# Performance work log

Measured on AMD Instinct MI355X. Metric: run time of the kernel, lower is better.

Reference implementation:

```python
import jax, jax.numpy as jnp
import numpy as np

N_NODES = 10000
N_EDGES = 320000
H = 256
L = 3
EPS = 1e-5


def _mlp2(x, w1, b1, w2, b2):
    # Linear -> ReLU -> Linear
    return jax.nn.relu(x @ w1 + b1) @ w2 + b2


def _layer_norm(x, g, b):
    mu = jnp.mean(x, axis=-1, keepdims=True)
    var = jnp.var(x, axis=-1, keepdims=True)
    return (x - mu) * jax.lax.rsqrt(var + EPS) * g + b


def setup_inputs() -> dict:
    key = jax.random.key(0)
    ks = jax.random.split(key, 24)
    s = 0.02
    inp = {
        "node_features": jax.random.normal(ks[0], (N_NODES, H), dtype=jnp.float32),
        "edge_index": jax.random.randint(ks[1], (2, N_EDGES), 0, N_NODES, dtype=jnp.int64),
        # node encoder (Linear 256->256, ReLU, Linear 256->256)
        "ne_w1": jax.random.normal(ks[2], (H, H), dtype=jnp.float32) * s,
        "ne_b1": jnp.zeros((H,), jnp.float32),
        "ne_w2": jax.random.normal(ks[3], (H, H), dtype=jnp.float32) * s,
        "ne_b2": jnp.zeros((H,), jnp.float32),
        # per-layer message MLP (2H->H, ReLU, H->H), stacked over L layers
        "msg_w1": jax.random.normal(ks[4], (L, 2 * H, H), dtype=jnp.float32) * s,
        "msg_b1": jnp.zeros((L, H), jnp.float32),
        "msg_w2": jax.random.normal(ks[5], (L, H, H), dtype=jnp.float32) * s,
        "msg_b2": jnp.zeros((L, H), jnp.float32),
        # per-layer update MLP (2H->H, ReLU, H->H)
        "upd_w1": jax.random.normal(ks[6], (L, 2 * H, H), dtype=jnp.float32) * s,
        "upd_b1": jnp.zeros((L, H), jnp.float32),
        "upd_w2": jax.random.normal(ks[7], (L, H, H), dtype=jnp.float32) * s,
        "upd_b2": jnp.zeros((L, H), jnp.float32),
        # per-layer LayerNorm
        "ln_g": jnp.ones((L, H), jnp.float32),
        "ln_b": jnp.zeros((L, H), jnp.float32),
        # readout MLP
        "ro_w1": jax.random.normal(ks[8], (H, H), dtype=jnp.float32) * s,
        "ro_b1": jnp.zeros((H,), jnp.float32),
        "ro_w2": jax.random.normal(ks[9], (H, H), dtype=jnp.float32) * s,
        "ro_b2": jnp.zeros((H,), jnp.float32),
    }
    return inp


def reference(node_features, edge_index, ne_w1, ne_b1, ne_w2, ne_b2,
              msg_w1, msg_b1, msg_w2, msg_b2,
              upd_w1, upd_b1, upd_w2, upd_b2,
              ln_g, ln_b, ro_w1, ro_b1, ro_w2, ro_b2):
    n_nodes = node_features.shape[0]
    src, dst = edge_index[0], edge_index[1]

    # node encoder
    x = _mlp2(node_features, ne_w1, ne_b1, ne_w2, ne_b2)  # [N, H]

    # message passing layers (edge_attr is unused in the original layer)
    for l in range(L):
        cat_e = jnp.concatenate([x[src], x[dst]], axis=-1)          # [E, 2H]
        messages = _mlp2(cat_e, msg_w1[l], msg_b1[l], msg_w2[l], msg_b2[l])  # [E, H]
        aggregated = jax.ops.segment_sum(messages, dst, num_segments=n_nodes)  # [N, H]
        cat_n = jnp.concatenate([x, aggregated], axis=-1)           # [N, 2H]
        updated = _mlp2(cat_n, upd_w1[l], upd_b1[l], upd_w2[l], upd_b2[l])
        x = _layer_norm(x + updated, ln_g[l], ln_b[l])

    # mean readout
    g = jnp.mean(x, axis=0)  # [H]
    return _mlp2(g, ro_w1, ro_b1, ro_w2, ro_b2)  # [H]
```

## Files before the change

### kernel.cpp

```cpp
#include <hip/hip_runtime.h>

#define NN 10000
#define NE 320000
#define HD 256
#define NL 3

typedef unsigned short ushort_t;
typedef __attribute__((ext_vector_type(8))) short bf16x8;
typedef __attribute__((ext_vector_type(4))) float f32x4;

#define MFMA __builtin_amdgcn_mfma_f32_16x16x32_bf16

#define WAITV(N) asm volatile("s_waitcnt vmcnt(" #N ")" ::: "memory")
#define SCHEDPIN() __builtin_amdgcn_sched_barrier(0)
#define LGKMBAR() do { asm volatile("s_waitcnt lgkmcnt(0)" ::: "memory"); \
                       __builtin_amdgcn_s_barrier(); __builtin_amdgcn_sched_barrier(0); } while (0)

__device__ __forceinline__ unsigned short f2bf(float x) {
    unsigned u = __float_as_uint(x);
    unsigned rounding = 0x7FFFu + ((u >> 16) & 1u);
    return (unsigned short)((u + rounding) >> 16);
}
__device__ __forceinline__ float bf2f(unsigned short u) {
    return __uint_as_float(((unsigned)u) << 16);
}
__device__ __forceinline__ int sw2(int col) { return (col & 3) ^ ((col >> 2) & 3); }
__device__ __forceinline__ void dma16(const void* g, void* l) {
    __builtin_amdgcn_global_load_lds(
        (const __attribute__((address_space(1))) unsigned int*)g,
        (__attribute__((address_space(3))) unsigned int*)l, 16, 0, 0);
}


__global__ void hist_deg(const int* __restrict__ dst, int* __restrict__ deg, int E) {
    int e = blockIdx.x * blockDim.x + threadIdx.x;
    if (e < E) atomicAdd(&deg[dst[e]], 1);
}

__global__ __launch_bounds__(1024) void scan_csr(const int* __restrict__ deg,
                                                 int* __restrict__ row_start,
                                                 int* __restrict__ cursor,
                                                 float* __restrict__ degf,
                                                 float* __restrict__ gsum, int n) {
    __shared__ int wsum[16];
    __shared__ int carry_s;
    int tid = threadIdx.x, lane = tid & 63, wid = tid >> 6;
    if (tid < HD) gsum[tid] = 0.f;
    if (tid == 0) carry_s = 0;
    __syncthreads();
    for (int base = 0; base < n; base += 1024) {
        int i = base + tid;
        int v = (i < n) ? deg[i] : 0;
        int s = v;
        #pragma unroll
        for (int off = 1; off < 64; off <<= 1) {
            int t = __shfl_up(s, off);
            if (lane >= off) s += t;
        }
        if (lane == 63) wsum[wid] = s;
        __syncthreads();
        if (wid == 0 && lane < 16) {
            int ws = wsum[lane];
            #pragma unroll
            for (int off = 1; off < 16; off <<= 1) {
                int t = __shfl_up(ws, off);
                if (lane >= off) ws += t;
            }
            wsum[lane] = ws;
        }
        __syncthreads();
        int carry = carry_s;
        int wpre = (wid > 0) ? wsum[wid - 1] : 0;
        int incl = carry + wpre + s;
        int excl = incl - v;
        if (i < n) { row_start[i] = excl; cursor[i] = excl; degf[i] = (float)v; }
        __syncthreads();
        if (tid == 1023) carry_s = incl;
        __syncthreads();
    }
    if (tid == 0) row_start[n] = carry_s;
}

__global__ void scatter_src(const int* __restrict__ src, const int* __restrict__ dst,
                            int* __restrict__ cursor, int* __restrict__ src_sorted, int E) {
    int e = blockIdx.x * blockDim.x + threadIdx.x;
    if (e < E) {
        int pos = atomicAdd(&cursor[dst[e]], 1);
        src_sorted[pos] = src[e];
    }
}


struct TDesc { const float* src; ushort_t* dst; int mode; };
struct TArgs { TDesc d[20]; };

__global__ __launch_bounds__(256) void conv_t(TArgs args) {
    __shared__ ushort_t tile[64][65];
    const float* src = args.d[blockIdx.y].src;
    ushort_t* dst = args.d[blockIdx.y].dst;
    int mode = args.d[blockIdx.y].mode;
    int t = blockIdx.x;
    int r0 = (t >> 2) * 64, c0 = (t & 3) * 64;
    int tid = threadIdx.x;
    int rr = tid >> 4, cc4 = (tid & 15) * 4;
    if (mode == 0) {
        #pragma unroll
        for (int i = 0; i < 4; ++i) {
            int r = r0 + rr + i * 16;
            float4 v = *(const float4*)(src + (size_t)r * HD + c0 + cc4);
            ushort4 o = { f2bf(v.x), f2bf(v.y), f2bf(v.z), f2bf(v.w) };
            *(ushort4*)(dst + (size_t)r * HD + c0 + cc4) = o;
        }
        return;
    }
    #pragma unroll
    for (int i = 0; i < 4; ++i) {
        int r = rr + i * 16;
        float4 v = *(const float4*)(src + (size_t)(r0 + r) * HD + c0 + cc4);
        tile[cc4 + 0][r] = f2bf(v.x);
        tile[cc4 + 1][r] = f2bf(v.y);
        tile[cc4 + 2][r] = f2bf(v.z);
        tile[cc4 + 3][r] = f2bf(v.w);
    }
    __syncthreads();
    #pragma unroll
    for (int i = 0; i < 4; ++i) {
        int c = rr + i * 16;
        ushort4 o = { tile[c][cc4], tile[c][cc4 + 1], tile[c][cc4 + 2], tile[c][cc4 + 3] };
        if (mode == 1) {
            *(ushort4*)(dst + (size_t)(c0 + c) * HD + r0 + cc4) = o;
        } else {
            int col = c0 + c;
            int k = r0 + cc4;
            int s = k >> 5, qv = (k >> 3) & 3;
            int slot = qv ^ sw2(col);
            *(ushort4*)(dst + (size_t)s * 8192 + col * 32 + slot * 8 + (k & 7)) = o;
        }
    }
}

__global__ __launch_bounds__(256) void cast_nf_tiled(const float* __restrict__ src,
                                                     ushort_t* __restrict__ dst) {
    int blk = blockIdx.x;
    int row = threadIdx.x >> 4, g = threadIdx.x & 15;
    const float* sp = src + ((size_t)blk * 16 + row) * HD + g * 16;
    ushort_t* dp = dst + (size_t)blk * 4096 + (g >> 1) * 512 + row * 32 + (g & 1) * 16;
    #pragma unroll
    for (int j = 0; j < 4; ++j) {
        float4 v = *(const float4*)(sp + j * 4);
        ushort4 o = { f2bf(v.x), f2bf(v.y), f2bf(v.z), f2bf(v.w) };
        *(ushort4*)(dp + j * 4) = o;
    }
}

__global__ __launch_bounds__(256) void bias_compose(const float* __restrict__ mb2,
                                                    const float* __restrict__ uw1,
                                                    float* __restrict__ out) {
    int l = blockIdx.x, c = threadIdx.x;
    const float* b2l = mb2 + (size_t)l * HD;
    const float* u1b = uw1 + (size_t)l * 2 * HD * HD + (size_t)HD * HD;
    float s = 0.f;
    for (int k = 0; k < HD; ++k) s += b2l[k] * u1b[(size_t)k * HD + c];
    out[(size_t)l * HD + c] = s;
}

__global__ __launch_bounds__(256) void gemm_w2u(
    const ushort_t* __restrict__ Abase, const ushort_t* __restrict__ Btbase,
    ushort_t* __restrict__ outBase)
{
    const ushort_t* A  = Abase  + (size_t)blockIdx.z * HD * HD;
    const ushort_t* Bt = Btbase + (size_t)blockIdx.z * HD * HD;
    ushort_t* outB     = outBase + (size_t)blockIdx.z * HD * HD;
    int tid = threadIdx.x;
    int wid = tid >> 6, lane = tid & 63;
    int wm = wid >> 1, wn = wid & 1;
    int row0 = blockIdx.x * 64 + wm * 32;
    int col0 = blockIdx.y * 64 + wn * 32;
    int lm = lane & 15, lk = (lane >> 4) * 8;
    f32x4 acc[2][2] = {};
    const ushort_t* a0p = A + (size_t)(row0 + lm) * HD + lk;
    const ushort_t* a1p = A + (size_t)(row0 + 16 + lm) * HD + lk;
    const ushort_t* b0p = Bt + (size_t)(col0 + lm) * HD + lk;
    const ushort_t* b1p = Bt + (size_t)(col0 + 16 + lm) * HD + lk;
    #pragma unroll
    for (int k0 = 0; k0 < HD; k0 += 32) {
        bf16x8 a0 = *(const bf16x8*)(a0p + k0);
        bf16x8 a1 = *(const bf16x8*)(a1p + k0);
        bf16x8 b0 = *(const bf16x8*)(b0p + k0);
        bf16x8 b1 = *(const bf16x8*)(b1p + k0);
        acc[0][0] = MFMA(a0, b0, acc[0][0], 0, 0, 0);
        acc[0][1] = MFMA(a0, b1, acc[0][1], 0, 0, 0);
        acc[1][0] = MFMA(a1, b0, acc[1][0], 0, 0, 0);
        acc[1][1] = MFMA(a1, b1, acc[1][1], 0, 0, 0);
    }
    int orow = (lane >> 4) * 4;
    #pragma unroll
    for (int mi = 0; mi < 2; ++mi)
        #pragma unroll
        for (int r = 0; r < 4; ++r) {
            int row = row0 + mi * 16 + orow + r;
            #pragma unroll
            for (int ni = 0; ni < 2; ++ni) {
                int col = col0 + ni * 16 + lm;
                int s = col >> 5, qv = (col >> 3) & 3;
                int slot = qv ^ sw2(row);
                outB[(size_t)s * 8192 + row * 32 + slot * 8 + (col & 7)] = f2bf(acc[mi][ni][r]);
            }
        }
}

__device__ __forceinline__ int swz(int row, int byte_in_row) {
    return row * 512 + (byte_in_row ^ ((row & 7) << 4));
}


__global__ __launch_bounds__(512, 4) void enc_pq(
    const ushort_t* __restrict__ Anf, const ushort_t* __restrict__ B1t,
    const ushort_t* __restrict__ B2t,
    const float* __restrict__ b1, const float* __restrict__ b2,
    const ushort_t* __restrict__ Pw1t, const ushort_t* __restrict__ Pw1b,
    const float* __restrict__ pqb1,
    float* __restrict__ xF, ushort_t* __restrict__ xB,
    ushort_t* __restrict__ P, float* __restrict__ Q, int M)
{
    __shared__ char wlds[8][2][2][2048];
    __shared__ char hid[16 * 512];
    int tid = threadIdx.x;
    int w = tid >> 6, lane = tid & 63;
    int lm = lane & 15, q = lane >> 4;
    int row0 = blockIdx.x * 16;
    int col0 = w * 32;
    int cA = col0 + lm, cB = col0 + 16 + lm;

    auto stageW = [&](const ushort_t* Wt, int s, int p, int m) {
        #pragma unroll
        for (int i = 0; i < 2; ++i)
            dma16((const char*)Wt + (size_t)s * 16384 + (col0 + 16 * i) * 64 + lane * 16,
                  wlds[w][p][m] + i * 1024);
    };
    auto readB = [&](int p, int m, int ni) -> bf16x8 {
        int col = col0 + 16 * ni + lm;
        int q2 = q ^ sw2(col);
        return *(const bf16x8*)(wlds[w][p][m] + ni * 1024 + lm * 64 + q2 * 16);
    };

    float b1v[2] = { b1[cA], b1[cB] };
    float b2v[2] = { b2[cA], b2[cB] };
    float pqv[2] = { pqb1[cA], pqb1[cB] };

    const ushort_t* ap = Anf + (size_t)blockIdx.x * 4096 + lm * 32 + q * 8;
    bf16x8 ax[2];
    #pragma unroll
    for (int s = 0; s < 2; ++s) {
        stageW(B1t, s, s, 0);
        ax[s] = *(const bf16x8*)(ap + s * 512);
        SCHEDPIN();
    }

    f32x4 acc[2] = {};
    #pragma unroll
    for (int j = 0; j < 8; ++j) {
        int p = j & 1;
        if (j < 7) { WAITV(3); } else { WAITV(0); }
        acc[0] = MFMA(ax[p], readB(p, 0, 0), acc[0], 0, 0, 0);
        acc[1] = MFMA(ax[p], readB(p, 0, 1), acc[1], 0, 0, 0);
        SCHEDPIN();
        if (j < 6) {
            stageW(B1t, j + 2, p, 0);
            ax[p] = *(const bf16x8*)(ap + (j + 2) * 512);
            SCHEDPIN();
        }
    }

    #pragma unroll
    for (int s = 0; s < 2; ++s) { stageW(B2t, s, s, 0); SCHEDPIN(); }
    #pragma unroll
    for (int ni = 0; ni < 2; ++ni) {
        int col = col0 + 16 * ni + lm;
        #pragma unroll
        for (int r = 0; r < 4; ++r) {
            int row = 4 * q + r;
            float v = fmaxf(acc[ni][r] + b1v[ni], 0.f);
            *(ushort_t*)(hid + swz(row, col * 2)) = f2bf(v);
        }
    }
    LGKMBAR();

    f32x4 acc2[2] = {};
    #pragma unroll
    for (int j = 0; j < 8; ++j) {
        int p = j & 1;
        if (j < 7) { WAITV(2); } else { WAITV(0); }
        int bk = (j * 32 + q * 8) * 2;
        bf16x8 a = *(const bf16x8*)(hid + swz(lm, bk));
        acc2[0] = MFMA(a, readB(p, 0, 0), acc2[0], 0, 0, 0);
        acc2[1] = MFMA(a, readB(p, 0, 1), acc2[1], 0, 0, 0);
        SCHEDPIN();
        if (j < 6) { stageW(B2t, j + 2, p, 0); SCHEDPIN(); }
    }

    #pragma unroll
    for (int s = 0; s < 2; ++s) {
        stageW(Pw1t, s, s, 0);
        stageW(Pw1b, s, s, 1);
        SCHEDPIN();
    }
    LGKMBAR();
    int tbase = blockIdx.x * 4096 + w * 512;
    #pragma unroll
    for (int ni = 0; ni < 2; ++ni) {
        int col = col0 + 16 * ni + lm;
        #pragma unroll
        for (int r = 0; r < 4; ++r) {
            int row = 4 * q + r;
            int grow = row0 + row;
            float v = acc2[ni][r] + b2v[ni];
            *(ushort_t*)(hid + swz(row, col * 2)) = f2bf(v);
            xF[(size_t)grow * HD + col] = v;
            xB[tbase + row * 32 + 16 * ni + lm] = f2bf(v);
        }
    }
    LGKMBAR();

    f32x4 aP[2] = {}, aQ[2] = {};
    #pragma unroll
    for (int j = 0; j < 8; ++j) {
        int p = j & 1;
        if (j < 7) { WAITV(4); } else { WAITV(0); }
        int bk = (j * 32 + q * 8) * 2;
        bf16x8 a = *(const bf16x8*)(hid + swz(lm, bk));
        #pragma unroll
        for (int ni = 0; ni < 2; ++ni) {
            aP[ni] = MFMA(a, readB(p, 0, ni), aP[ni], 0, 0, 0);
            aQ[ni] = MFMA(a, readB(p, 1, ni), aQ[ni], 0, 0, 0);
        }
        SCHEDPIN();
        if (j < 6) {
            stageW(Pw1t, j + 2, p, 0);
            stageW(Pw1b, j + 2, p, 1);
            SCHEDPIN();
        }
    }
    #pragma unroll
    for (int r = 0; r < 4; ++r) {
        int grow = row0 + 4 * q + r;
        #pragma unroll
        for (int ni = 0; ni < 2; ++ni) {
            int col = col0 + 16 * ni + lm;
            P[(size_t)grow * HD + col] = f2bf(aP[ni][r]);
            Q[(size_t)grow * HD + col] = aQ[ni][r] + pqv[ni];
        }
    }
}


__global__ __launch_bounds__(256) void edge_agg(
    const ushort_t* __restrict__ Pb, const float* __restrict__ Qf,
    const int* __restrict__ row_start, const int* __restrict__ srcs,
    ushort_t* __restrict__ HaggT)
{
    int node = blockIdx.x * 4 + (threadIdx.x >> 6);
    int lane = threadIdx.x & 63;
    int c4 = lane * 4;
    float4 qb = *(const float4*)(Qf + (size_t)node * HD + c4);
    float4 acc = {0.f, 0.f, 0.f, 0.f};
    int j = row_start[node], e = row_start[node + 1];
    for (; j + 8 <= e; j += 8) {
        ushort4 p[8];
        #pragma unroll
        for (int u = 0; u < 8; ++u) {
            int s = srcs[j + u];
            p[u] = *(const ushort4*)(Pb + (size_t)s * HD + c4);
        }
        #pragma unroll
        for (int u = 0; u < 8; ++u) {
            acc.x += fmaxf(bf2f(p[u].x) + qb.x, 0.f);
            acc.y += fmaxf(bf2f(p[u].y) + qb.y, 0.f);
            acc.z += fmaxf(bf2f(p[u].z) + qb.z, 0.f);
            acc.w += fmaxf(bf2f(p[u].w) + qb.w, 0.f);
        }
    }
    for (; j < e; ++j) {
        int s0 = srcs[j];
        ushort4 p0 = *(const ushort4*)(Pb + (size_t)s0 * HD + c4);
        acc.x += fmaxf(bf2f(p0.x) + qb.x, 0.f);
        acc.y += fmaxf(bf2f(p0.y) + qb.y, 0.f);
        acc.z += fmaxf(bf2f(p0.z) + qb.z, 0.f);
        acc.w += fmaxf(bf2f(p0.w) + qb.w, 0.f);
    }
    ushort4 o = { f2bf(acc.x), f2bf(acc.y), f2bf(acc.z), f2bf(acc.w) };
    int tidx = (node >> 4) * 4096 + (c4 >> 5) * 512 + (node & 15) * 32 + (c4 & 31);
    *(ushort4*)(HaggT + tidx) = o;
}


__global__ __launch_bounds__(512, 4) void upd_ln(
    const ushort_t* __restrict__ xb, const ushort_t* __restrict__ Hb,
    const ushort_t* __restrict__ B1t, const ushort_t* __restrict__ B2t,
    const ushort_t* __restrict__ B3t,
    const float* __restrict__ degf,
    const float* __restrict__ b1, const float* __restrict__ bias2,
    const float* __restrict__ b3,
    const float* __restrict__ g, const float* __restrict__ bb,
    const ushort_t* __restrict__ Pw1t, const ushort_t* __restrict__ Pw1b,
    const float* __restrict__ pqb1,
    float* __restrict__ gsum,
    float* __restrict__ xF, ushort_t* __restrict__ xB,
    ushort_t* __restrict__ P, float* __restrict__ Q, int M)
{
    __shared__ char wlds[8][2][2][2048];
    __shared__ char hid[16 * 512];
    __shared__ float sS[8][16], sQ[8][16], muv[16], ivv[16];

    int tid = threadIdx.x;
    int w = tid >> 6, lane = tid & 63;
    int lm = lane & 15, q = lane >> 4;
    int row0 = blockIdx.x * 16;
    int col0 = w * 32;
    int cA = col0 + lm, cB = col0 + 16 + lm;

    auto stageW = [&](const ushort_t* Wt, int s, int p, int m) {
        #pragma unroll
        for (int i = 0; i < 2; ++i)
            dma16((const char*)Wt + (size_t)s * 16384 + (col0 + 16 * i) * 64 + lane * 16,
                  wlds[w][p][m] + i * 1024);
    };
    auto readB = [&](int p, int m, int ni) -> bf16x8 {
        int col = col0 + 16 * ni + lm;
        int q2 = q ^ sw2(col);
        return *(const bf16x8*)(wlds[w][p][m] + ni * 1024 + lm * 64 + q2 * 16);
    };

    const ushort_t* xp = xb + (size_t)blockIdx.x * 4096 + lm * 32 + q * 8;
    const ushort_t* hp = Hb + (size_t)blockIdx.x * 4096 + lm * 32 + q * 8;
    bf16x8 ax[2], ah[2];
    #pragma unroll
    for (int s = 0; s < 2; ++s) {
        stageW(B1t, s, s, 0);
        stageW(B2t, s, s, 1);
        ax[s] = *(const bf16x8*)(xp + s * 512);
        ah[s] = *(const bf16x8*)(hp + s * 512);
        SCHEDPIN();
    }

    float b1v[2] = { b1[cA], b1[cB] };
    float bzv[2] = { bias2[cA], bias2[cB] };
    float b3v[2] = { b3[cA], b3[cB] };
    float gv[2]  = { g[cA],  g[cB]  };
    float bbv[2] = { bb[cA], bb[cB] };
    float pqv[2] = { Pw1t ? pqb1[cA] : 0.f, Pw1t ? pqb1[cB] : 0.f };
    float dgv[4], res[2][4];
    #pragma unroll
    for (int r = 0; r < 4; ++r) {
        int row = 4 * q + r;
        dgv[r] = degf[row0 + row];
        res[0][r] = xF[(size_t)(row0 + row) * HD + cA];
        res[1][r] = xF[(size_t)(row0 + row) * HD + cB];
    }

    f32x4 acc[2] = {};
    #pragma unroll
    for (int j = 0; j < 8; ++j) {
        int p = j & 1;
        if (j < 7) { WAITV(6); } else { WAITV(0); }
        #pragma unroll
        for (int ni = 0; ni < 2; ++ni) {
            acc[ni] = MFMA(ax[p], readB(p, 0, ni), acc[ni], 0, 0, 0);
            acc[ni] = MFMA(ah[p], readB(p, 1, ni), acc[ni], 0, 0, 0);
        }
        SCHEDPIN();
        if (j < 6) {
            stageW(B1t, j + 2, p, 0);
            stageW(B2t, j + 2, p, 1);
            ax[p] = *(const bf16x8*)(xp + (j + 2) * 512);
            ah[p] = *(const bf16x8*)(hp + (j + 2) * 512);
            SCHEDPIN();
        }
    }

    #pragma unroll
    for (int s = 0; s < 2; ++s) { stageW(B3t, s, s, 0); SCHEDPIN(); }
    #pragma unroll
    for (int r = 0; r < 4; ++r) {
        int row = 4 * q + r;
        #pragma unroll
        for (int ni = 0; ni < 2; ++ni) {
            int col = col0 + 16 * ni + lm;
            float v = fmaxf(acc[ni][r] + b1v[ni] + dgv[r] * bzv[ni], 0.f);
            *(ushort_t*)(hid + swz(row, col * 2)) = f2bf(v);
        }
    }
    LGKMBAR();

    f32x4 acc2[2] = {};
    #pragma unroll
    for (int j = 0; j < 8; ++j) {
        int p = j & 1;
        if (j < 7) { WAITV(2); } else { WAITV(0); }
        int bk = (j * 32 + q * 8) * 2;
        bf16x8 a = *(const bf16x8*)(hid + swz(lm, bk));
        acc2[0] = MFMA(a, readB(p, 0, 0), acc2[0], 0, 0, 0);
        acc2[1] = MFMA(a, readB(p, 0, 1), acc2[1], 0, 0, 0);
        SCHEDPIN();
        if (j < 6) { stageW(B3t, j + 2, p, 0); SCHEDPIN(); }
    }

    if (Pw1t) {
        #pragma unroll
        for (int s = 0; s < 2; ++s) {
            stageW(Pw1t, s, s, 0);
            stageW(Pw1b, s, s, 1);
            SCHEDPIN();
        }
    }
    #pragma unroll
    for (int r = 0; r < 4; ++r) {
        float s = 0.f, qq = 0.f;
        #pragma unroll
        for (int ni = 0; ni < 2; ++ni) {
            float v = acc2[ni][r] + b3v[ni] + res[ni][r];
            acc2[ni][r] = v;
            s += v; qq += v * v;
        }
        #pragma unroll
        for (int off = 1; off < 16; off <<= 1) {
            s += __shfl_xor(s, off);
            qq += __shfl_xor(qq, off);
        }
        if (lm == 0) {
            int row = 4 * q + r;
            sS[w][row] = s; sQ[w][row] = qq;
        }
    }
    LGKMBAR();
    if (tid < 16) {
        float s = 0.f, qq = 0.f;
        #pragma unroll
        for (int i = 0; i < 8; ++i) { s += sS[i][tid]; qq += sQ[i][tid]; }
        float mu = s * (1.0f / HD);
        float var = qq * (1.0f / HD) - mu * mu;
        muv[tid] = mu;
        ivv[tid] = rsqrtf(var + 1e-5f);
    }
    LGKMBAR();
    float csum[2] = {0.f, 0.f};
    int tbase = blockIdx.x * 4096 + w * 512;
    #pragma unroll
    for (int r = 0; r < 4; ++r) {
        int row = 4 * q + r;
        int grow = row0 + row;
        float mu = muv[row], iv = ivv[row];
        #pragma unroll
        for (int ni = 0; ni < 2; ++ni) {
            int col = col0 + 16 * ni + lm;
            float o = (acc2[ni][r] - mu) * iv * gv[ni] + bbv[ni];
            *(ushort_t*)(hid + swz(row, col * 2)) = f2bf(o);
            xF[(size_t)grow * HD + col] = o;
            xB[tbase + row * 32 + 16 * ni + lm] = f2bf(o);
            csum[ni] += o;
        }
    }
    if (gsum) {
        #pragma unroll
        for (int ni = 0; ni < 2; ++ni) {
            float s = csum[ni];
            s += __shfl_xor(s, 16);
            s += __shfl_xor(s, 32);
            if (q == 0) atomicAdd(&gsum[col0 + 16 * ni + lm], s);
        }
    }

    if (Pw1t) {
        LGKMBAR();
        f32x4 aP[2] = {}, aQ[2] = {};
        #pragma unroll
        for (int j = 0; j < 8; ++j) {
            int p = j & 1;
            if (j < 7) { WAITV(4); } else { WAITV(0); }
            int bk = (j * 32 + q * 8) * 2;
            bf16x8 a = *(const bf16x8*)(hid + swz(lm, bk));
            #pragma unroll
            for (int ni = 0; ni < 2; ++ni) {
                aP[ni] = MFMA(a, readB(p, 0, ni), aP[ni], 0, 0, 0);
                aQ[ni] = MFMA(a, readB(p, 1, ni), aQ[ni], 0, 0, 0);
            }
            SCHEDPIN();
            if (j < 6) {
                stageW(Pw1t, j + 2, p, 0);
                stageW(Pw1b, j + 2, p, 1);
                SCHEDPIN();
            }
        }
        #pragma unroll
        for (int r = 0; r < 4; ++r) {
            int grow = row0 + 4 * q + r;
            #pragma unroll
            for (int ni = 0; ni < 2; ++ni) {
                int col = col0 + 16 * ni + lm;
                P[(size_t)grow * HD + col] = f2bf(aP[ni][r]);
                Q[(size_t)grow * HD + col] = aQ[ni][r] + pqv[ni];
            }
        }
    }
}


__global__ __launch_bounds__(256) void readout_mlp(
    const float* __restrict__ gsum,
    const float* __restrict__ w1, const float* __restrict__ b1,
    const float* __restrict__ w2, const float* __restrict__ b2,
    float* __restrict__ out, float invn)
{
    __shared__ float gl[HD], h1[HD];
    int c = threadIdx.x;
    gl[c] = gsum[c] * invn;
    __syncthreads();
    float a = b1[c];
    for (int k = 0; k < HD; ++k) a += gl[k] * w1[k * HD + c];
    h1[c] = fmaxf(a, 0.f);
    __syncthreads();
    float o = b2[c];
    for (int k = 0; k < HD; ++k) o += h1[k] * w2[k * HD + c];
    out[c] = o;
}


extern "C" void kernel_launch(void* const* d_in, const int* in_sizes, int n_in,
                              void* d_out, int out_size, void* d_ws, size_t ws_size,
                              hipStream_t stream) {
    const float* nf    = (const float*)d_in[0];
    const int*   ei    = (const int*)d_in[1];
    const float* ne_w1 = (const float*)d_in[2];
    const float* ne_b1 = (const float*)d_in[3];
    const float* ne_w2 = (const float*)d_in[4];
    const float* ne_b2 = (const float*)d_in[5];
    const float* mw1   = (const float*)d_in[6];
    const float* mb1   = (const float*)d_in[7];
    const float* mw2   = (const float*)d_in[8];
    const float* mb2   = (const float*)d_in[9];
    const float* uw1   = (const float*)d_in[10];
    const float* ub1   = (const float*)d_in[11];
    const float* uw2   = (const float*)d_in[12];
    const float* ub2   = (const float*)d_in[13];
    const float* lng   = (const float*)d_in[14];
    const float* lnb   = (const float*)d_in[15];
    const float* rw1   = (const float*)d_in[16];
    const float* rb1   = (const float*)d_in[17];
    const float* rw2   = (const float*)d_in[18];
    const float* rb2   = (const float*)d_in[19];

    const int* e_src = ei;
    const int* e_dst = ei + NE;

    char* w = (char*)d_ws;
    size_t off = 0;
    auto alloc = [&](size_t bytes) -> void* {
        void* p = w + off;
        off = (off + bytes + 255) & ~(size_t)255;
        return p;
    };
    const size_t NF32 = (size_t)NN * HD * sizeof(float);
    const size_t NF16 = (size_t)NN * HD * sizeof(ushort_t);
    const size_t WM16 = (size_t)HD * HD * sizeof(ushort_t);

    float* x    = (float*)alloc(NF32);
    float* Qf   = (float*)alloc(NF32);
    float* gsum = (float*)alloc(HD * sizeof(float));
    float* degf = (float*)alloc(NN * sizeof(float));
    float* b2u1 = (float*)alloc(NL * HD * sizeof(float));

    ushort_t* nfT   = (ushort_t*)alloc(NF16);
    ushort_t* xb    = (ushort_t*)alloc(NF16);
    ushort_t* Pb    = (ushort_t*)alloc(NF16);
    ushort_t* Haggb = (ushort_t*)alloc(NF16);
    ushort_t* neT1  = (ushort_t*)alloc(WM16);
    ushort_t* neT2  = (ushort_t*)alloc(WM16);
    ushort_t* w1tT  = (ushort_t*)alloc(NL * WM16);
    ushort_t* w1bT  = (ushort_t*)alloc(NL * WM16);
    ushort_t* u1tT  = (ushort_t*)alloc(NL * WM16);
    ushort_t* u1bT  = (ushort_t*)alloc(NL * WM16);
    ushort_t* u2T   = (ushort_t*)alloc(NL * WM16);
    ushort_t* w2uT  = (ushort_t*)alloc(NL * WM16);
    ushort_t* w2rmb = (ushort_t*)alloc(NL * WM16);

    int* deg       = (int*)alloc(NN * sizeof(int));
    int* row_start = (int*)alloc((NN + 1) * sizeof(int));
    int* cursor    = (int*)alloc(NN * sizeof(int));
    int* srcs      = (int*)alloc(NE * sizeof(int));

    hipMemsetAsync(deg, 0, NN * sizeof(int), stream);

    hist_deg<<<(NE + 255) / 256, 256, 0, stream>>>(e_dst, deg, NE);
    scan_csr<<<1, 1024, 0, stream>>>(deg, row_start, cursor, degf, gsum, NN);
    scatter_src<<<(NE + 255) / 256, 256, 0, stream>>>(e_src, e_dst, cursor, srcs, NE);

    TArgs ta;
    ta.d[0] = { ne_w1, neT1, 2 };
    ta.d[1] = { ne_w2, neT2, 2 };
    for (int l = 0; l < NL; ++l) {
        const float* w1l = mw1 + (size_t)l * 2 * HD * HD;
        const float* u1l = uw1 + (size_t)l * 2 * HD * HD;
        ta.d[2 + l]  = { w1l,                       w1tT + (size_t)l * HD * HD, 2 };
        ta.d[5 + l]  = { w1l + (size_t)HD * HD,     w1bT + (size_t)l * HD * HD, 2 };
        ta.d[8 + l]  = { u1l,                       u1tT + (size_t)l * HD * HD, 2 };
        ta.d[11 + l] = { u1l + (size_t)HD * HD,     u1bT + (size_t)l * HD * HD, 1 };
        ta.d[14 + l] = { uw2 + (size_t)l * HD * HD, u2T + (size_t)l * HD * HD, 2 };
        ta.d[17 + l] = { mw2 + (size_t)l * HD * HD, w2rmb + (size_t)l * HD * HD, 0 };
    }
    conv_t<<<dim3(16, 20), 256, 0, stream>>>(ta);
    cast_nf_tiled<<<NN / 16, 256, 0, stream>>>(nf, nfT);
    bias_compose<<<NL, 256, 0, stream>>>(mb2, uw1, b2u1);
    gemm_w2u<<<dim3(4, 4, NL), 256, 0, stream>>>(u1bT, w2rmb, w2uT);

    enc_pq<<<NN / 16, 512, 0, stream>>>(nfT, neT1, neT2, ne_b1, ne_b2,
                                        w1tT, w1bT, mb1, x, xb, Pb, Qf, NN);

    for (int l = 0; l < NL; ++l) {
        edge_agg<<<NN / 4, 256, 0, stream>>>(Pb, Qf, row_start, srcs, Haggb);
        int nl = l + 1;
        const ushort_t* pw1t = (nl < NL) ? w1tT + (size_t)nl * HD * HD : nullptr;
        const ushort_t* pw1b = (nl < NL) ? w1bT + (size_t)nl * HD * HD : nullptr;
        const float*    pqb1 = (nl < NL) ? mb1 + (size_t)nl * HD : nullptr;
        float* gs = (l == NL - 1) ? gsum : nullptr;
        upd_ln<<<NN / 16, 512, 0, stream>>>(
            xb, Haggb, u1tT + (size_t)l * HD * HD, w2uT + (size_t)l * HD * HD,
            u2T + (size_t)l * HD * HD, degf,
            ub1 + (size_t)l * HD, b2u1 + (size_t)l * HD, ub2 + (size_t)l * HD,
            lng + (size_t)l * HD, lnb + (size_t)l * HD,
            pw1t, pw1b, pqb1, gs, x, xb, Pb, Qf, NN);
    }

    readout_mlp<<<1, 256, 0, stream>>>(gsum, rw1, rb1, rw2, rb2, (float*)d_out, 1.0f / NN);
}
```

Before: 285.3 us.

## Load weight fragments directly into registers instead of staging via LDS DMA

The node encoder and update kernels no longer stage weight slices through per-wave LDS buffers with global_load_lds and manual vmcnt waits. Each lane now loads its bf16x8 weight fragment straight from global memory into registers, double-buffered, and leaves scheduling to the compiler. The transposed weight layout drops its XOR swizzle to match, and row reads are clamped to M-1. This removes LDS capacity pressure and the explicit wait/barrier pinning, but relies on L2/cache hits and compiler scheduling to hide global load latency.

```diff
diff --git a/kernel.cpp b/kernel.cpp
--- a/kernel.cpp
+++ b/kernel.cpp
@@ -11,8 +11,6 @@
 
 #define MFMA __builtin_amdgcn_mfma_f32_16x16x32_bf16
 
-#define WAITV(N) asm volatile("s_waitcnt vmcnt(" #N ")" ::: "memory")
-#define SCHEDPIN() __builtin_amdgcn_sched_barrier(0)
 #define LGKMBAR() do { asm volatile("s_waitcnt lgkmcnt(0)" ::: "memory"); \
                        __builtin_amdgcn_s_barrier(); __builtin_amdgcn_sched_barrier(0); } while (0)
 
@@ -23,12 +21,6 @@
 }
 __device__ __forceinline__ float bf2f(unsigned short u) {
     return __uint_as_float(((unsigned)u) << 16);
-}
-__device__ __forceinline__ int sw2(int col) { return (col & 3) ^ ((col >> 2) & 3); }
-__device__ __forceinline__ void dma16(const void* g, void* l) {
-    __builtin_amdgcn_global_load_lds(
-        (const __attribute__((address_space(1))) unsigned int*)g,
-        (__attribute__((address_space(3))) unsigned int*)l, 16, 0, 0);
 }
 
 
@@ -132,9 +124,7 @@
         } else {
             int col = c0 + c;
             int k = r0 + cc4;
-            int s = k >> 5, qv = (k >> 3) & 3;
-            int slot = qv ^ sw2(col);
-            *(ushort4*)(dst + (size_t)s * 8192 + col * 32 + slot * 8 + (k & 7)) = o;
+            *(ushort4*)(dst + (size_t)(k >> 5) * 8192 + col * 32 + (k & 31)) = o;
         }
     }
 }
@@ -202,9 +192,7 @@
             #pragma unroll
             for (int ni = 0; ni < 2; ++ni) {
                 int col = col0 + ni * 16 + lm;
-                int s = col >> 5, qv = (col >> 3) & 3;
-                int slot = qv ^ sw2(row);
-                outB[(size_t)s * 8192 + row * 32 + slot * 8 + (col & 7)] = f2bf(acc[mi][ni][r]);
+                outB[(size_t)(col >> 5) * 8192 + row * 32 + (col & 31)] = f2bf(acc[mi][ni][r]);
             }
         }
 }
@@ -223,7 +211,6 @@
     float* __restrict__ xF, ushort_t* __restrict__ xB,
     ushort_t* __restrict__ P, float* __restrict__ Q, int M)
 {
-    __shared__ char wlds[8][2][2][2048];
     __shared__ char hid[16 * 512];
     int tid = threadIdx.x;
     int w = tid >> 6, lane = tid & 63;
@@ -231,49 +218,38 @@
     int row0 = blockIdx.x * 16;
     int col0 = w * 32;
     int cA = col0 + lm, cB = col0 + 16 + lm;
-
-    auto stageW = [&](const ushort_t* Wt, int s, int p, int m) {
-        #pragma unroll
-        for (int i = 0; i < 2; ++i)
-            dma16((const char*)Wt + (size_t)s * 16384 + (col0 + 16 * i) * 64 + lane * 16,
-                  wlds[w][p][m] + i * 1024);
+    size_t boff = (size_t)(col0 + lm) * 64 + q * 16;
+
+    auto ldW = [&](const ushort_t* Wt, int s, int ni) -> bf16x8 {
+        return *(const bf16x8*)((const char*)Wt + (size_t)s * 16384 + boff + ni * 1024);
     };
-    auto readB = [&](int p, int m, int ni) -> bf16x8 {
-        int col = col0 + 16 * ni + lm;
-        int q2 = q ^ sw2(col);
-        return *(const bf16x8*)(wlds[w][p][m] + ni * 1024 + lm * 64 + q2 * 16);
-    };
-
+    const ushort_t* ap = Anf + (size_t)blockIdx.x * 4096 + lm * 32 + q * 8;
+
+    bf16x8 wb[2][2], axr[2];
+    #pragma unroll
+    for (int s = 0; s < 2; ++s) {
+        wb[s][0] = ldW(B1t, s, 0); wb[s][1] = ldW(B1t, s, 1);
+        axr[s] = *(const bf16x8*)(ap + s * 512);
+    }
     float b1v[2] = { b1[cA], b1[cB] };
     float b2v[2] = { b2[cA], b2[cB] };
-    float pqv[2] = { pqb1[cA], pqb1[cB] };
-
-    const ushort_t* ap = Anf + (size_t)blockIdx.x * 4096 + lm * 32 + q * 8;
-    bf16x8 ax[2];
-    #pragma unroll
-    for (int s = 0; s < 2; ++s) {
-        stageW(B1t, s, s, 0);
-        ax[s] = *(const bf16x8*)(ap + s * 512);
-        SCHEDPIN();
-    }
 
     f32x4 acc[2] = {};
     #pragma unroll
     for (int j = 0; j < 8; ++j) {
         int p = j & 1;
-        if (j < 7) { WAITV(3); } else { WAITV(0); }
-        acc[0] = MFMA(ax[p], readB(p, 0, 0), acc[0], 0, 0, 0);
-        acc[1] = MFMA(ax[p], readB(p, 0, 1), acc[1], 0, 0, 0);
-        SCHEDPIN();
+        acc[0] = MFMA(axr[p], wb[p][0], acc[0], 0, 0, 0);
+        acc[1] = MFMA(axr[p], wb[p][1], acc[1], 0, 0, 0);
         if (j < 6) {
-            stageW(B1t, j + 2, p, 0);
-            ax[p] = *(const bf16x8*)(ap + (j + 2) * 512);
-            SCHEDPIN();
-        }
-    }
-
-    #pragma unroll
-    for (int s = 0; s < 2; ++s) { stageW(B2t, s, s, 0); SCHEDPIN(); }
+            wb[p][0] = ldW(B1t, j + 2, 0); wb[p][1] = ldW(B1t, j + 2, 1);
+            axr[p] = *(const bf16x8*)(ap + (j + 2) * 512);
+        }
+    }
+
+    bf16x8 vw[2][2];
+    #pragma unroll
+    for (int s = 0; s < 2; ++s) { vw[s][0] = ldW(B2t, s, 0); vw[s][1] = ldW(B2t, s, 1); }
+
     #pragma unroll
     for (int ni = 0; ni < 2; ++ni) {
         int col = col0 + 16 * ni + lm;
@@ -290,21 +266,20 @@
     #pragma unroll
     for (int j = 0; j < 8; ++j) {
         int p = j & 1;
-        if (j < 7) { WAITV(2); } else { WAITV(0); }
         int bk = (j * 32 + q * 8) * 2;
         bf16x8 a = *(const bf16x8*)(hid + swz(lm, bk));
-        acc2[0] = MFMA(a, readB(p, 0, 0), acc2[0], 0, 0, 0);
-        acc2[1] = MFMA(a, readB(p, 0, 1), acc2[1], 0, 0, 0);
-        SCHEDPIN();
-        if (j < 6) { stageW(B2t, j + 2, p, 0); SCHEDPIN(); }
-    }
-
+        acc2[0] = MFMA(a, vw[p][0], acc2[0], 0, 0, 0);
+        acc2[1] = MFMA(a, vw[p][1], acc2[1], 0, 0, 0);
+        if (j < 6) { vw[p][0] = ldW(B2t, j + 2, 0); vw[p][1] = ldW(B2t, j + 2, 1); }
+    }
+
+    bf16x8 pw[2][2], qw[2][2];
     #pragma unroll
     for (int s = 0; s < 2; ++s) {
-        stageW(Pw1t, s, s, 0);
-        stageW(Pw1b, s, s, 1);
-        SCHEDPIN();
-    }
+        pw[s][0] = ldW(Pw1t, s, 0); pw[s][1] = ldW(Pw1t, s, 1);
+        qw[s][0] = ldW(Pw1b, s, 0); qw[s][1] = ldW(Pw1b, s, 1);
+    }
+    float pqv[2] = { pqb1[cA], pqb1[cB] };
     LGKMBAR();
     int tbase = blockIdx.x * 4096 + w * 512;
     #pragma unroll
@@ -326,19 +301,15 @@
     #pragma unroll
     for (int j = 0; j < 8; ++j) {
         int p = j & 1;
-        if (j < 7) { WAITV(4); } else { WAITV(0); }
         int bk = (j * 32 + q * 8) * 2;
         bf16x8 a = *(const bf16x8*)(hid + swz(lm, bk));
-        #pragma unroll
-        for (int ni = 0; ni < 2; ++ni) {
-            aP[ni] = MFMA(a, readB(p, 0, ni), aP[ni], 0, 0, 0);
-            aQ[ni] = MFMA(a, readB(p, 1, ni), aQ[ni], 0, 0, 0);
-        }
-        SCHEDPIN();
+        aP[0] = MFMA(a, pw[p][0], aP[0], 0, 0, 0);
+        aP[1] = MFMA(a, pw[p][1], aP[1], 0, 0, 0);
+        aQ[0] = MFMA(a, qw[p][0], aQ[0], 0, 0, 0);
+        aQ[1] = MFMA(a, qw[p][1], aQ[1], 0, 0, 0);
         if (j < 6) {
-            stageW(Pw1t, j + 2, p, 0);
-            stageW(Pw1b, j + 2, p, 1);
-            SCHEDPIN();
+            pw[p][0] = ldW(Pw1t, j + 2, 0); pw[p][1] = ldW(Pw1t, j + 2, 1);
+            qw[p][0] = ldW(Pw1b, j + 2, 0); qw[p][1] = ldW(Pw1b, j + 2, 1);
         }
     }
     #pragma unroll
@@ -408,78 +379,56 @@
     float* __restrict__ xF, ushort_t* __restrict__ xB,
     ushort_t* __restrict__ P, float* __restrict__ Q, int M)
 {
-    __shared__ char wlds[8][2][2][2048];
     __shared__ char hid[16 * 512];
     __shared__ float sS[8][16], sQ[8][16], muv[16], ivv[16];
-
     int tid = threadIdx.x;
     int w = tid >> 6, lane = tid & 63;
     int lm = lane & 15, q = lane >> 4;
     int row0 = blockIdx.x * 16;
     int col0 = w * 32;
     int cA = col0 + lm, cB = col0 + 16 + lm;
-
-    auto stageW = [&](const ushort_t* Wt, int s, int p, int m) {
-        #pragma unroll
-        for (int i = 0; i < 2; ++i)
-            dma16((const char*)Wt + (size_t)s * 16384 + (col0 + 16 * i) * 64 + lane * 16,
-                  wlds[w][p][m] + i * 1024);
+    size_t boff = (size_t)(col0 + lm) * 64 + q * 16;
+
+    auto ldW = [&](const ushort_t* Wt, int s, int ni) -> bf16x8 {
+        return *(const bf16x8*)((const char*)Wt + (size_t)s * 16384 + boff + ni * 1024);
     };
-    auto readB = [&](int p, int m, int ni) -> bf16x8 {
-        int col = col0 + 16 * ni + lm;
-        int q2 = q ^ sw2(col);
-        return *(const bf16x8*)(wlds[w][p][m] + ni * 1024 + lm * 64 + q2 * 16);
-    };
-
     const ushort_t* xp = xb + (size_t)blockIdx.x * 4096 + lm * 32 + q * 8;
     const ushort_t* hp = Hb + (size_t)blockIdx.x * 4096 + lm * 32 + q * 8;
-    bf16x8 ax[2], ah[2];
+
+    bf16x8 wb[2][2][2], axr[2], ahr[2];
     #pragma unroll
     for (int s = 0; s < 2; ++s) {
-        stageW(B1t, s, s, 0);
-        stageW(B2t, s, s, 1);
-        ax[s] = *(const bf16x8*)(xp + s * 512);
-        ah[s] = *(const bf16x8*)(hp + s * 512);
-        SCHEDPIN();
-    }
-
+        wb[s][0][0] = ldW(B1t, s, 0); wb[s][0][1] = ldW(B1t, s, 1);
+        wb[s][1][0] = ldW(B2t, s, 0); wb[s][1][1] = ldW(B2t, s, 1);
+        axr[s] = *(const bf16x8*)(xp + s * 512);
+        ahr[s] = *(const bf16x8*)(hp + s * 512);
+    }
     float b1v[2] = { b1[cA], b1[cB] };
     float bzv[2] = { bias2[cA], bias2[cB] };
-    float b3v[2] = { b3[cA], b3[cB] };
-    float gv[2]  = { g[cA],  g[cB]  };
-    float bbv[2] = { bb[cA], bb[cB] };
-    float pqv[2] = { Pw1t ? pqb1[cA] : 0.f, Pw1t ? pqb1[cB] : 0.f };
-    float dgv[4], res[2][4];
-    #pragma unroll
-    for (int r = 0; r < 4; ++r) {
-        int row = 4 * q + r;
-        dgv[r] = degf[row0 + row];
-        res[0][r] = xF[(size_t)(row0 + row) * HD + cA];
-        res[1][r] = xF[(size_t)(row0 + row) * HD + cB];
-    }
+    float dgv[4];
+    #pragma unroll
+    for (int r = 0; r < 4; ++r) dgv[r] = degf[min(row0 + 4 * q + r, M - 1)];
 
     f32x4 acc[2] = {};
     #pragma unroll
     for (int j = 0; j < 8; ++j) {
         int p = j & 1;
-        if (j < 7) { WAITV(6); } else { WAITV(0); }
-        #pragma unroll
-        for (int ni = 0; ni < 2; ++ni) {
-            acc[ni] = MFMA(ax[p], readB(p, 0, ni), acc[ni], 0, 0, 0);
-            acc[ni] = MFMA(ah[p], readB(p, 1, ni), acc[ni], 0, 0, 0);
-        }
-        SCHEDPIN();
+        acc[0] = MFMA(axr[p], wb[p][0][0], acc[0], 0, 0, 0);
+        acc[0] = MFMA(ahr[p], wb[p][1][0], acc[0], 0, 0, 0);
+        acc[1] = MFMA(axr[p], wb[p][0][1], acc[1], 0, 0, 0);
+        acc[1] = MFMA(ahr[p], wb[p][1][1], acc[1], 0, 0, 0);
         if (j < 6) {
-            stageW(B1t, j + 2, p, 0);
-            stageW(B2t, j + 2, p, 1);
-            ax[p] = *(const bf16x8*)(xp + (j + 2) * 512);
-            ah[p] = *(const bf16x8*)(hp + (j + 2) * 512);
-            SCHEDPIN();
-        }
-    }
-
-    #pragma unroll
-    for (int s = 0; s < 2; ++s) { stageW(B3t, s, s, 0); SCHEDPIN(); }
+            wb[p][0][0] = ldW(B1t, j + 2, 0); wb[p][0][1] = ldW(B1t, j + 2, 1);
+            wb[p][1][0] = ldW(B2t, j + 2, 0); wb[p][1][1] = ldW(B2t, j + 2, 1);
+            axr[p] = *(const bf16x8*)(xp + (j + 2) * 512);
+            ahr[p] = *(const bf16x8*)(hp + (j + 2) * 512);
+        }
+    }
+
+    bf16x8 uw[2][2];
+    #pragma unroll
+    for (int s = 0; s < 2; ++s) { uw[s][0] = ldW(B3t, s, 0); uw[s][1] = ldW(B3t, s, 1); }
+
     #pragma unroll
     for (int r = 0; r < 4; ++r) {
         int row = 4 * q + r;
@@ -492,27 +441,39 @@
     }
     LGKMBAR();
 
+    float b3v[2] = { b3[cA], b3[cB] };
+    float gv[2]  = { g[cA],  g[cB]  };
+    float bbv[2] = { bb[cA], bb[cB] };
+    float res[2][4];
+    #pragma unroll
+    for (int r = 0; r < 4; ++r) {
+        int gr = min(row0 + 4 * q + r, M - 1);
+        res[0][r] = xF[(size_t)gr * HD + cA];
+        res[1][r] = xF[(size_t)gr * HD + cB];
+    }
+
     f32x4 acc2[2] = {};
     #pragma unroll
     for (int j = 0; j < 8; ++j) {
         int p = j & 1;
-        if (j < 7) { WAITV(2); } else { WAITV(0); }
         int bk = (j * 32 + q * 8) * 2;
         bf16x8 a = *(const bf16x8*)(hid + swz(lm, bk));
-        acc2[0] = MFMA(a, readB(p, 0, 0), acc2[0], 0, 0, 0);
-        acc2[1] = MFMA(a, readB(p, 0, 1), acc2[1], 0, 0, 0);
-        SCHEDPIN();
-        if (j < 6) { stageW(B3t, j + 2, p, 0); SCHEDPIN(); }
-    }
-
+        acc2[0] = MFMA(a, uw[p][0], acc2[0], 0, 0, 0);
+        acc2[1] = MFMA(a, uw[p][1], acc2[1], 0, 0, 0);
+        if (j < 6) { uw[p][0] = ldW(B3t, j + 2, 0); uw[p][1] = ldW(B3t, j + 2, 1); }
+    }
+
+    bf16x8 pw[2][2], qw[2][2];
+    float pqv[2] = { 0.f, 0.f };
     if (Pw1t) {
         #pragma unroll
         for (int s = 0; s < 2; ++s) {
-            stageW(Pw1t, s, s, 0);
-            stageW(Pw1b, s, s, 1);
-            SCHEDPIN();
-        }
-    }
+            pw[s][0] = ldW(Pw1t, s, 0); pw[s][1] = ldW(Pw1t, s, 1);
+            qw[s][0] = ldW(Pw1b, s, 0); qw[s][1] = ldW(Pw1b, s, 1);
+        }
+        pqv[0] = pqb1[cA]; pqv[1] = pqb1[cB];
+    }
+
     #pragma unroll
     for (int r = 0; r < 4; ++r) {
         float s = 0.f, qq = 0.f;
@@ -576,19 +537,15 @@
         #pragma unroll
         for (int j = 0; j < 8; ++j) {
             int p = j & 1;
-            if (j < 7) { WAITV(4); } else { WAITV(0); }
             int bk = (j * 32 + q * 8) * 2;
             bf16x8 a = *(const bf16x8*)(hid + swz(lm, bk));
-            #pragma unroll
-            for (int ni = 0; ni < 2; ++ni) {
-                aP[ni] = MFMA(a, readB(p, 0, ni), aP[ni], 0, 0, 0);
-                aQ[ni] = MFMA(a, readB(p, 1, ni), aQ[ni], 0, 0, 0);
-            }
-            SCHEDPIN();
+            aP[0] = MFMA(a, pw[p][0], aP[0], 0, 0, 0);
+            aP[1] = MFMA(a, pw[p][1], aP[1], 0, 0, 0);
+            aQ[0] = MFMA(a, qw[p][0], aQ[0], 0, 0, 0);
+            aQ[1] = MFMA(a, qw[p][1], aQ[1], 0, 0, 0);
             if (j < 6) {
-                stageW(Pw1t, j + 2, p, 0);
-                stageW(Pw1b, j + 2, p, 1);
-                SCHEDPIN();
+                pw[p][0] = ldW(Pw1t, j + 2, 0); pw[p][1] = ldW(Pw1t, j + 2, 1);
+                qw[p][0] = ldW(Pw1b, j + 2, 0); qw[p][1] = ldW(Pw1b, j + 2, 1);
             }
         }
         #pragma unroll
```

Measured after the change: 307.2 us. +7.7%, slower.
